# Kernel tuning notes

Measured on AMD Instinct MI355X. Metric: run time of the kernel, lower is better.

The kernel has to match this reference:

```python
import jax, jax.numpy as jnp
import numpy as np

N_NODES = 50000
N_GRAPHS = 64
IN_DIM, HIDDEN, OUT_DIM = 2063, 256, 128
E_L, E_G = 800000, 1600000


def setup_inputs() -> dict:
    key = jax.random.key(0)
    ks = jax.random.split(key, 16)
    x = jax.random.normal(ks[0], (N_NODES, IN_DIM), dtype=jnp.float32)
    edge_index_l = jax.random.randint(ks[1], (2, E_L), 0, N_NODES, dtype=jnp.int64)
    edge_index_g = jax.random.randint(ks[2], (2, E_G), 0, N_NODES, dtype=jnp.int64)
    batch = jnp.sort(jax.random.randint(ks[3], (N_NODES,), 0, N_GRAPHS, dtype=jnp.int64))

    def glorot(k, shape):
        scale = jnp.sqrt(2.0 / (shape[0] + shape[1])).astype(jnp.float32)
        return jax.random.normal(k, shape, dtype=jnp.float32) * scale

    return {
        "x": x,
        "edge_index_l": edge_index_l,
        "edge_index_g": edge_index_g,
        "batch": batch,
        "W_l1": glorot(ks[4], (IN_DIM, HIDDEN)), "b_l1": jnp.zeros((HIDDEN,), jnp.float32),
        "W_l2": glorot(ks[5], (HIDDEN, OUT_DIM)), "b_l2": jnp.zeros((OUT_DIM,), jnp.float32),
        "W_g1": glorot(ks[6], (IN_DIM, HIDDEN)), "b_g1": jnp.zeros((HIDDEN,), jnp.float32),
        "W_g2": glorot(ks[7], (HIDDEN, OUT_DIM)), "b_g2": jnp.zeros((OUT_DIM,), jnp.float32),
        "W_fuse": glorot(ks[8], (2 * OUT_DIM, OUT_DIM)), "b_fuse": jnp.zeros((OUT_DIM,), jnp.float32),
    }


def gcn_conv(x, edge_index, W, b):
    # PyG GCNConv: add self loops, symmetric D^{-1/2}(A+I)D^{-1/2} normalization,
    # linear transform then scatter-add aggregation at target nodes.
    n = x.shape[0]
    loops = jnp.arange(n, dtype=edge_index.dtype)
    src = jnp.concatenate([edge_index[0], loops])
    dst = jnp.concatenate([edge_index[1], loops])
    deg = jax.ops.segment_sum(jnp.ones_like(dst, dtype=x.dtype), dst, num_segments=n)
    dinv = jax.lax.rsqrt(deg)  # deg >= 1 due to self loops
    norm = dinv[src] * dinv[dst]  # [E+n]
    h = x @ W  # [n, out]
    msg = h[src] * norm[:, None]  # gather + scale
    return jax.ops.segment_sum(msg, dst, num_segments=n) + b


def global_mean_pool(x, batch, num_graphs):
    sums = jax.ops.segment_sum(x, batch, num_segments=num_graphs)
    cnt = jax.ops.segment_sum(jnp.ones((x.shape[0],), x.dtype), batch, num_segments=num_graphs)
    return sums / jnp.maximum(cnt, 1.0)[:, None]


def reference(x, edge_index_l, edge_index_g, batch,
              W_l1, b_l1, W_l2, b_l2, W_g1, b_g1, W_g2, b_g2, W_fuse, b_fuse):
    # dropout is identity in eval mode
    xl = jax.nn.relu(gcn_conv(x, edge_index_l, W_l1, b_l1))
    xl = gcn_conv(xl, edge_index_l, W_l2, b_l2)
    xl = global_mean_pool(xl, batch, N_GRAPHS)

    xg = jax.nn.relu(gcn_conv(x, edge_index_g, W_g1, b_g1))
    xg = gcn_conv(xg, edge_index_g, W_g2, b_g2)
    xg = global_mean_pool(xg, batch, N_GRAPHS)

    out = jnp.concatenate([xl, xg], axis=1)  # [G, 2*out_dim]
    return jax.nn.relu(out @ W_fuse + b_fuse)
```

## Files before the change

kernel.cpp:

```cpp
#include <hip/hip_runtime.h>
#include <hip/hip_bf16.h>
#include <cstdint>
#include <cstddef>


#define N_NODES 50000
#define N_GRAPHS 64
#define IN_DIM 2063
#define HIDDEN 256
#define OUT_DIM 128
#define EDGES_L 800000
#define EDGES_G 1600000
#define HCOLS 512
#define KPAD 2112
#define MPAD 50048
#define GBM 64
#define NT (KPAD / 32)
#define PCH 256
#define NCHUNK ((N_NODES + PCH - 1) / PCH)

#define QUARTER 12544
#define SL_L 64
#define SL_G 128
#define EPS 12500
#define HBLOCKS (4 * (SL_L + SL_G))

typedef __attribute__((ext_vector_type(8))) __bf16 bf16x8;
typedef __attribute__((ext_vector_type(4))) float f32x4;

__device__ __forceinline__ float bf2f(unsigned short u) {
  union { unsigned int i; float f; } c; c.i = ((unsigned int)u) << 16; return c.f;
}
__device__ __forceinline__ unsigned short f2bf(float f) {
  __hip_bfloat16 h = __float2bfloat16(f);
  return *reinterpret_cast<unsigned short*>(&h);
}

__global__ void k_cvt_w(const float* __restrict__ Wl, const float* __restrict__ Wg,
                        unsigned short* __restrict__ Wt) {
  int i = blockIdx.x * blockDim.x + threadIdx.x;
  if (i >= HCOLS * KPAD) return;
  int n = i / KPAD;
  int k = i - n * KPAD;
  float v = 0.f;
  if (k < IN_DIM) {
    v = (n < HIDDEN) ? Wl[(size_t)k * HIDDEN + n] : Wg[(size_t)k * HIDDEN + (n - HIDDEN)];
  }
  Wt[(size_t)n * KPAD + k] = f2bf(v);
}

__launch_bounds__(256)
__global__ void k_hist(const int* __restrict__ dstL, const int* __restrict__ dstG,
                       int* __restrict__ partL, int* __restrict__ partG) {
  __shared__ int hist[QUARTER];
  const int i = blockIdx.x;
  const int* __restrict__ dst;
  int slice, q;
  int* __restrict__ part;
  if (i < 4 * SL_L) {
    slice = i >> 2; q = i & 3;
    dst = dstL;
    part = partL + (size_t)(slice * 4 + q) * QUARTER;
  } else {
    int j = i - 4 * SL_L;
    slice = j >> 2; q = j & 3;
    dst = dstG;
    part = partG + (size_t)(slice * 4 + q) * QUARTER;
  }
  for (int t = threadIdx.x; t < QUARTER; t += 256) hist[t] = 0;
  __syncthreads();
  const int e0 = slice * EPS;
  const int qbase = q * QUARTER;
  for (int e = e0 + threadIdx.x; e < e0 + EPS; e += 256) {
    int d = dst[e] - qbase;
    if ((unsigned)d < QUARTER) atomicAdd(&hist[d], 1);
  }
  __syncthreads();
  for (int t = threadIdx.x; t < QUARTER; t += 256) part[t] = hist[t];
}

__global__ void k_prefix(int* __restrict__ partL, int* __restrict__ partG,
                         const int* __restrict__ batch, int* __restrict__ degL,
                         int* __restrict__ degG, float* __restrict__ dinvL,
                         float* __restrict__ dinvG, float* __restrict__ cL,
                         float* __restrict__ cG) {
  int t = blockIdx.x * blockDim.x + threadIdx.x;
  if (t >= 8 * QUARTER) return;
  const int b = t / (4 * QUARTER);
  const int n = t - b * 4 * QUARTER;
  const int q = n / QUARTER, loc = n - q * QUARTER;
  const int NS = b ? SL_G : SL_L;
  int* p = (b ? partG : partL) + (size_t)q * QUARTER + loc;
  int run = 0;
  for (int s = 0; s < NS; s++) {
    int* pp = p + (size_t)s * 4 * QUARTER;
    int v = *pp;
    *pp = run;
    run += v;
  }
  if (n < N_NODES) {
    float d = 1.0f / sqrtf((float)(run + 1));
    if (b == 0) {
      degL[n] = run; dinvL[n] = d; cL[(size_t)n * 64 + batch[n]] = d * d;
    } else {
      degG[n] = run; dinvG[n] = d; cG[(size_t)n * 64 + batch[n]] = d * d;
    }
  }
}

__global__ void k_scan1(const int* __restrict__ degL, const int* __restrict__ degG,
                        int* __restrict__ rowL, int* __restrict__ rowG,
                        const int* __restrict__ batch, int* __restrict__ start) {
  if (blockIdx.x >= 2) {
    int n = (blockIdx.x - 2) * 1024 + threadIdx.x;
    if (n >= N_NODES) return;
    int bn = batch[n];
    int bp = n ? batch[n - 1] : -1;
    for (int g = bp + 1; g <= bn; g++) start[g] = n;
    if (n == N_NODES - 1)
      for (int g = bn + 1; g <= N_GRAPHS; g++) start[g] = N_NODES;
    return;
  }
  __shared__ int part[1024];
  const int t = threadIdx.x;
  const int* __restrict__ deg = blockIdx.x ? degG : degL;
  int* __restrict__ row = blockIdx.x ? rowG : rowL;
  const int c0 = t * 49;
  int s = 0;
  for (int j = 0; j < 49; j++) {
    int idx = c0 + j;
    s += (idx < N_NODES) ? deg[idx] : 0;
  }
  part[t] = s;
  __syncthreads();
  for (int ofs = 1; ofs < 1024; ofs <<= 1) {
    int v = (t >= ofs) ? part[t - ofs] : 0;
    __syncthreads();
    part[t] += v;
    __syncthreads();
  }
  int run = (t > 0) ? part[t - 1] : 0;
  for (int j = 0; j < 49; j++) {
    int idx = c0 + j;
    if (idx < N_NODES) { row[idx] = run; run += deg[idx]; }
  }
  if (t == 1023) row[N_NODES] = part[1023];
}

__launch_bounds__(256)
__global__ void k_scatter2(const int* __restrict__ srcL, const int* __restrict__ dstL,
                           const int* __restrict__ srcG, const int* __restrict__ dstG,
                           const int* __restrict__ partL, const int* __restrict__ partG,
                           const int* __restrict__ rowL, const int* __restrict__ rowG,
                           const float* __restrict__ dinvL, const float* __restrict__ dinvG,
                           const int* __restrict__ batch, int2* __restrict__ erL,
                           int2* __restrict__ erG, float* __restrict__ cL,
                           float* __restrict__ cG) {
  __shared__ int hist[QUARTER];
  const int i = blockIdx.x;
  const int *src, *dst, *part, *row;
  const float* dinv;
  int2* er;
  float* c;
  int slice, q;
  if (i < 4 * SL_L) {
    slice = i >> 2; q = i & 3;
    src = srcL; dst = dstL; row = rowL; dinv = dinvL; er = erL; c = cL;
    part = partL + (size_t)(slice * 4 + q) * QUARTER;
  } else {
    int j = i - 4 * SL_L;
    slice = j >> 2; q = j & 3;
    src = srcG; dst = dstG; row = rowG; dinv = dinvG; er = erG; c = cG;
    part = partG + (size_t)(slice * 4 + q) * QUARTER;
  }
  for (int t = threadIdx.x; t < QUARTER; t += 256) hist[t] = 0;
  __syncthreads();
  const int e0 = slice * EPS;
  const int qbase = q * QUARTER;
  for (int e = e0 + threadIdx.x; e < e0 + EPS; e += 256) {
    int d = dst[e];
    int loc = d - qbase;
    if ((unsigned)loc < QUARTER) {
      int s = src[e];
      int rank = atomicAdd(&hist[loc], 1);
      int pos = row[d] + part[loc] + rank;
      float nrm = dinv[s] * dinv[d];
      er[pos] = make_int2(s, __float_as_int(nrm));
      atomicAdd(&c[(size_t)s * 64 + batch[d]], nrm);
    }
  }
}

__launch_bounds__(256)
__global__ void k_mfma_gemm(const float* __restrict__ X,
                            const unsigned short* __restrict__ Wt,
                            unsigned short* __restrict__ H) {
  __shared__ __align__(16) char lds[2 * 4096 + 2 * 32768];
  char* const Ab0 = lds;
  char* const Ab1 = lds + 4096;
  char* const Bb0 = lds + 8192;
  char* const Bb1 = lds + 8192 + 32768;
  const int tid = threadIdx.x;
  const int lane = tid & 63;
  const int wave = tid >> 6;
  const int brow = blockIdx.x * GBM;

  const int ar = tid >> 2;
  const int ach = tid & 3;
  const int askew = (ar >> 1) & 3;
  const int asrc = (ach ^ askew) * 8;
  const int arow_g = brow + ar;
  const bool aok = arow_g < N_NODES;
  const float* __restrict__ Arow = X + (size_t)arow_g * IN_DIM;

  const int fr = lane & 15;
  const int fq = lane >> 4;

  f32x4 acc[4][8];
  const f32x4 zero = {0.f, 0.f, 0.f, 0.f};
#pragma unroll
  for (int m = 0; m < 4; m++)
#pragma unroll
    for (int n = 0; n < 8; n++) acc[m][n] = zero;

#pragma unroll
  for (int i = 0; i < 8; i++) {
    const int s = i * 256 + tid;
    const int row = s >> 2, cch = s & 3;
    const unsigned short* g = Wt + (size_t)row * KPAD + ((cch ^ ((row >> 1) & 3)) * 8);
    __builtin_amdgcn_global_load_lds(
        (const __attribute__((address_space(1))) void*)g,
        (__attribute__((address_space(3))) void*)(Bb0 + (i * 256 + wave * 64) * 16),
        16, 0, 0);
  }
  float a[8];
#pragma unroll
  for (int j = 0; j < 8; j++) a[j] = aok ? Arow[asrc + j] : 0.f;
  {
    uint u0 = (uint)f2bf(a[0]) | ((uint)f2bf(a[1]) << 16);
    uint u1 = (uint)f2bf(a[2]) | ((uint)f2bf(a[3]) << 16);
    uint u2 = (uint)f2bf(a[4]) | ((uint)f2bf(a[5]) << 16);
    uint u3 = (uint)f2bf(a[6]) | ((uint)f2bf(a[7]) << 16);
    *(uint4*)(Ab0 + tid * 16) = make_uint4(u0, u1, u2, u3);
  }
  __syncthreads();

  for (int t = 0; t < NT; ++t) {
    const int k0 = t * 32;
    char* const Acur = (t & 1) ? Ab1 : Ab0;
    char* const Bcur = (t & 1) ? Bb1 : Bb0;
    char* const Anxt = (t & 1) ? Ab0 : Ab1;
    char* const Bnxt = (t & 1) ? Bb0 : Bb1;

    if (t + 1 < NT) {
      const int kn = k0 + 32;
#pragma unroll
      for (int i = 0; i < 8; i++) {
        const int s = i * 256 + tid;
        const int row = s >> 2, cch = s & 3;
        const unsigned short* g = Wt + (size_t)row * KPAD + kn + ((cch ^ ((row >> 1) & 3)) * 8);
        __builtin_amdgcn_global_load_lds(
            (const __attribute__((address_space(1))) void*)g,
            (__attribute__((address_space(3))) void*)(Bnxt + (i * 256 + wave * 64) * 16),
            16, 0, 0);
      }
      const int kb = kn + asrc;
      if (aok) {
        if (kb + 7 < IN_DIM) {
#pragma unroll
          for (int j = 0; j < 8; j++) a[j] = Arow[kb + j];
        } else {
#pragma unroll
          for (int j = 0; j < 8; j++) a[j] = (kb + j < IN_DIM) ? Arow[kb + j] : 0.f;
        }
      }
    }

    {
      bf16x8 bv[8];
#pragma unroll
      for (int n = 0; n < 8; n++) {
        const int row = wave * 128 + n * 16 + fr;
        bv[n] = *(const bf16x8*)(Bcur + row * 64 + ((fq ^ ((row >> 1) & 3)) * 16));
      }
#pragma unroll
      for (int m = 0; m < 4; m++) {
        const int row = m * 16 + fr;
        bf16x8 av = *(const bf16x8*)(Acur + row * 64 + ((fq ^ ((row >> 1) & 3)) * 16));
#pragma unroll
        for (int n = 0; n < 8; n++)
          acc[m][n] = __builtin_amdgcn_mfma_f32_16x16x32_bf16(av, bv[n], acc[m][n], 0, 0, 0);
      }
    }

    if (t + 1 < NT) {
      uint u0 = (uint)f2bf(a[0]) | ((uint)f2bf(a[1]) << 16);
      uint u1 = (uint)f2bf(a[2]) | ((uint)f2bf(a[3]) << 16);
      uint u2 = (uint)f2bf(a[4]) | ((uint)f2bf(a[5]) << 16);
      uint u3 = (uint)f2bf(a[6]) | ((uint)f2bf(a[7]) << 16);
      *(uint4*)(Anxt + tid * 16) = make_uint4(u0, u1, u2, u3);
    }
    __syncthreads();
  }

#pragma unroll
  for (int m = 0; m < 4; m++) {
    const int r0 = brow + m * 16 + fq * 4;
#pragma unroll
    for (int n = 0; n < 8; n++) {
      const int col = wave * 128 + n * 16 + fr;
#pragma unroll
      for (int j = 0; j < 4; j++) {
        int r = r0 + j;
        if (r < N_NODES) H[(size_t)r * HCOLS + col] = f2bf(acc[m][n][j]);
      }
    }
  }
}

__global__ void k_agg(const unsigned short* __restrict__ h,
                      const float* __restrict__ dinvL, const float* __restrict__ dinvG,
                      const int* __restrict__ rowL, const int* __restrict__ rowG,
                      const int2* __restrict__ erL, const int2* __restrict__ erG,
                      const float* __restrict__ biasL, const float* __restrict__ biasG,
                      unsigned short* __restrict__ xl) {
  const int br = blockIdx.y;
  const int node = blockIdx.x * 4 + (threadIdx.x >> 6);
  const int lane = threadIdx.x & 63;
  const float* __restrict__ dinv = br ? dinvG : dinvL;
  const int* __restrict__ rp = br ? rowG : rowL;
  const int2* __restrict__ er = br ? erG : erL;
  const float* __restrict__ bias = br ? biasG : biasL;
  const int off = br ? 256 : 0;
  const size_t lcol = off + lane * 4;

  float di = dinv[node];
  float w0 = di * di;
  ushort4 u = *(const ushort4*)(h + (size_t)node * HCOLS + lcol);
  float a0 = w0 * bf2f(u.x), a1 = w0 * bf2f(u.y), a2 = w0 * bf2f(u.z), a3 = w0 * bf2f(u.w);

  int e = rp[node];
  const int e1 = rp[node + 1];
  for (; e + 8 <= e1; e += 8) {
    int2 r[8];
    ushort4 v[8];
#pragma unroll
    for (int j = 0; j < 8; j++) r[j] = er[e + j];
#pragma unroll
    for (int j = 0; j < 8; j++)
      v[j] = *(const ushort4*)(h + (size_t)r[j].x * HCOLS + lcol);
#pragma unroll
    for (int j = 0; j < 8; j++) {
      float w = __int_as_float(r[j].y);
      a0 = fmaf(w, bf2f(v[j].x), a0);
      a1 = fmaf(w, bf2f(v[j].y), a1);
      a2 = fmaf(w, bf2f(v[j].z), a2);
      a3 = fmaf(w, bf2f(v[j].w), a3);
    }
  }
  for (; e + 4 <= e1; e += 4) {
    int2 r[4];
    ushort4 v[4];
#pragma unroll
    for (int j = 0; j < 4; j++) r[j] = er[e + j];
#pragma unroll
    for (int j = 0; j < 4; j++)
      v[j] = *(const ushort4*)(h + (size_t)r[j].x * HCOLS + lcol);
#pragma unroll
    for (int j = 0; j < 4; j++) {
      float w = __int_as_float(r[j].y);
      a0 = fmaf(w, bf2f(v[j].x), a0);
      a1 = fmaf(w, bf2f(v[j].y), a1);
      a2 = fmaf(w, bf2f(v[j].z), a2);
      a3 = fmaf(w, bf2f(v[j].w), a3);
    }
  }
  for (; e < e1; e++) {
    int2 r = er[e];
    float w = __int_as_float(r.y);
    ushort4 v = *(const ushort4*)(h + (size_t)r.x * HCOLS + lcol);
    a0 = fmaf(w, bf2f(v.x), a0);
    a1 = fmaf(w, bf2f(v.y), a1);
    a2 = fmaf(w, bf2f(v.z), a2);
    a3 = fmaf(w, bf2f(v.w), a3);
  }
  float4 b = *(const float4*)(bias + lane * 4);
  ushort4 o;
  o.x = f2bf(fmaxf(a0 + b.x, 0.f));
  o.y = f2bf(fmaxf(a1 + b.y, 0.f));
  o.z = f2bf(fmaxf(a2 + b.z, 0.f));
  o.w = f2bf(fmaxf(a3 + b.w, 0.f));
  *(ushort4*)(xl + (size_t)node * HCOLS + lcol) = o;
}

__launch_bounds__(256)
__global__ void k_pool2(const unsigned short* __restrict__ xl,
                        const float* __restrict__ cL, const float* __restrict__ cG,
                        float* __restrict__ Spart) {
  __shared__ float cs[64][64];
  const int t = threadIdx.x;
  const int chunk = blockIdx.x;
  const int br = blockIdx.y;
  const float* __restrict__ C = br ? cG : cL;
  const int xoff = br ? 256 : 0;
  const int n0 = chunk * PCH;
  float acc[64];
#pragma unroll
  for (int g = 0; g < 64; g++) acc[g] = 0.f;

  for (int tile = 0; tile < PCH; tile += 64) {
    const int base = n0 + tile;
    __syncthreads();
#pragma unroll
    for (int i = 0; i < 16; i++) {
      int idx = i * 256 + t;
      int nn = idx >> 6, gg = idx & 63;
      int node = base + nn;
      cs[nn][gg] = (node < N_NODES) ? C[(size_t)node * 64 + gg] : 0.f;
    }
    __syncthreads();
    for (int nn = 0; nn < 64; nn++) {
      int node = base + nn;
      float v = (node < N_NODES) ? bf2f(xl[(size_t)node * HCOLS + xoff + t]) : 0.f;
#pragma unroll
      for (int g4 = 0; g4 < 16; g4++) {
        float4 cv = *(const float4*)&cs[nn][g4 * 4];
        acc[g4 * 4 + 0] = fmaf(cv.x, v, acc[g4 * 4 + 0]);
        acc[g4 * 4 + 1] = fmaf(cv.y, v, acc[g4 * 4 + 1]);
        acc[g4 * 4 + 2] = fmaf(cv.z, v, acc[g4 * 4 + 2]);
        acc[g4 * 4 + 3] = fmaf(cv.w, v, acc[g4 * 4 + 3]);
      }
    }
  }
  float* sp = Spart + ((size_t)br * NCHUNK + chunk) * 16384 + t;
#pragma unroll
  for (int g = 0; g < 64; g++) sp[g * 256] = acc[g];
}

__global__ void k_pool_reduce(const float* __restrict__ Spart, float* __restrict__ S) {
  int i = blockIdx.x * blockDim.x + threadIdx.x;
  if (i >= 2 * 16384) return;
  int br = i >> 14, idx = i & 16383;
  const float* p = Spart + (size_t)br * NCHUNK * 16384 + idx;
  float s = 0.f;
  for (int ch = 0; ch < NCHUNK; ch++) s += p[(size_t)ch * 16384];
  S[i] = s;
}

__global__ void k_final(const float* __restrict__ S,
                        const float* __restrict__ Wl2, const float* __restrict__ bl2,
                        const float* __restrict__ Wg2, const float* __restrict__ bg2,
                        const float* __restrict__ Wf, const float* __restrict__ bf,
                        const int* __restrict__ start, float* __restrict__ out) {
  __shared__ float pl[OUT_DIM], pg[OUT_DIM];
  int g = blockIdx.x, t = threadIdx.x;
  float invc = 1.0f / fmaxf((float)(start[g + 1] - start[g]), 1.0f);
  const float* Sl = S + (size_t)g * HIDDEN;
  const float* Sg = S + (size_t)N_GRAPHS * HIDDEN + (size_t)g * HIDDEN;
  float al = 0.f, ag = 0.f;
  for (int k = 0; k < HIDDEN; k++) {
    al = fmaf(Sl[k], Wl2[k * OUT_DIM + t], al);
    ag = fmaf(Sg[k], Wg2[k * OUT_DIM + t], ag);
  }
  pl[t] = al * invc + bl2[t];
  pg[t] = ag * invc + bg2[t];
  __syncthreads();
  float o = bf[t];
  for (int j = 0; j < OUT_DIM; j++) {
    o = fmaf(pl[j], Wf[j * OUT_DIM + t], o);
    o = fmaf(pg[j], Wf[(OUT_DIM + j) * OUT_DIM + t], o);
  }
  out[(size_t)g * OUT_DIM + t] = fmaxf(o, 0.f);
}

extern "C" void kernel_launch(void* const* d_in, const int* in_sizes, int n_in,
                              void* d_out, int out_size, void* d_ws, size_t ws_size,
                              hipStream_t stream) {
  const float* x = (const float*)d_in[0];
  const int* el = (const int*)d_in[1];
  const int* eg = (const int*)d_in[2];
  const int* batch = (const int*)d_in[3];
  const float* Wl1 = (const float*)d_in[4];
  const float* bl1 = (const float*)d_in[5];
  const float* Wl2 = (const float*)d_in[6];
  const float* bl2 = (const float*)d_in[7];
  const float* Wg1 = (const float*)d_in[8];
  const float* bg1 = (const float*)d_in[9];
  const float* Wg2 = (const float*)d_in[10];
  const float* bg2 = (const float*)d_in[11];
  const float* Wf = (const float*)d_in[12];
  const float* bf = (const float*)d_in[13];
  float* out = (float*)d_out;
  char* ws = (char*)d_ws;

  const size_t NPAD = 200192;
  size_t off = 0;
  float* c_l = (float*)(ws + off); off += (size_t)N_NODES * 64 * 4;
  float* c_g = (float*)(ws + off); off += (size_t)N_NODES * 64 * 4;
  const size_t zero_bytes = off;
  int* start = (int*)(ws + off); off += 512;
  float* S = (float*)(ws + off); off += (size_t)2 * N_GRAPHS * HIDDEN * 4;
  int* deg_l = (int*)(ws + off); off += NPAD;
  int* deg_g = (int*)(ws + off); off += NPAD;
  float* dinv_l = (float*)(ws + off); off += NPAD;
  float* dinv_g = (float*)(ws + off); off += NPAD;
  int* row_l = (int*)(ws + off); off += NPAD;
  int* row_g = (int*)(ws + off); off += NPAD;
  int* partL = (int*)(ws + off); off += (size_t)SL_L * 4 * QUARTER * 4;
  int* partG = (int*)(ws + off); off += (size_t)SL_G * 4 * QUARTER * 4;
  int2* er_l = (int2*)(ws + off); off += (size_t)EDGES_L * 8;
  int2* er_g = (int2*)(ws + off); off += (size_t)EDGES_G * 8;
  unsigned short* Wt = (unsigned short*)(ws + off); off += (size_t)HCOLS * KPAD * 2;
  unsigned short* h = (unsigned short*)(ws + off); off += (size_t)N_NODES * HCOLS * 2;
  unsigned short* xl = (unsigned short*)(ws + off); off += (size_t)N_NODES * HCOLS * 2;
  float* Spart = (float*)partL;

  const int* srcL = el;
  const int* dstL = el + EDGES_L;
  const int* srcG = eg;
  const int* dstG = eg + EDGES_G;

  hipMemsetAsync(ws, 0, zero_bytes, stream);

  k_cvt_w<<<(HCOLS * KPAD + 255) / 256, 256, 0, stream>>>(Wl1, Wg1, Wt);

  k_hist<<<HBLOCKS, 256, 0, stream>>>(dstL, dstG, partL, partG);
  k_prefix<<<(8 * QUARTER + 255) / 256, 256, 0, stream>>>(partL, partG, batch, deg_l, deg_g,
                                                          dinv_l, dinv_g, c_l, c_g);
  k_scan1<<<51, 1024, 0, stream>>>(deg_l, deg_g, row_l, row_g, batch, start);
  k_scatter2<<<HBLOCKS, 256, 0, stream>>>(srcL, dstL, srcG, dstG, partL, partG, row_l, row_g,
                                          dinv_l, dinv_g, batch, er_l, er_g, c_l, c_g);

  k_mfma_gemm<<<MPAD / GBM, 256, 0, stream>>>(x, Wt, h);

  dim3 agrid(N_NODES / 4, 2);
  k_agg<<<agrid, 256, 0, stream>>>(h, dinv_l, dinv_g, row_l, row_g, er_l, er_g, bl1, bg1, xl);

  dim3 pgrid(NCHUNK, 2);
  k_pool2<<<pgrid, 256, 0, stream>>>(xl, c_l, c_g, Spart);
  k_pool_reduce<<<(2 * 16384 + 255) / 256, 256, 0, stream>>>(Spart, S);

  k_final<<<N_GRAPHS, OUT_DIM, 0, stream>>>(S, Wl2, bl2, Wg2, bg2, Wf, bf, start, out);
}
```

Baseline: 950.8 us.

## Merge edge scatter and MFMA GEMM into one interleaved heterogeneous launch

Fuses the CSR edge-scatter kernel and the bf16 MFMA feature GEMM into a single launch. The first 2*HBLOCKS blocks alternate between scatter and GEMM work, and the remaining blocks do GEMM, so the latency-bound scatter atomics can overlap with the compute-bound GEMM on the same CUs. The scatter blocks now reserve the GEMM's larger LDS allocation, which can reduce their occupancy. The scatter path and the GEMM path also share one register budget.

```diff
diff --git a/kernel.cpp b/kernel.cpp
--- a/kernel.cpp
+++ b/kernel.cpp
@@ -15,6 +15,7 @@
 #define KPAD 2112
 #define MPAD 50048
 #define GBM 64
+#define NGB (MPAD / GBM)
 #define NT (KPAD / 32)
 #define PCH 256
 #define NCHUNK ((N_NODES + PCH - 1) / PCH)
@@ -148,54 +149,66 @@
 }
 
 __launch_bounds__(256)
-__global__ void k_scatter2(const int* __restrict__ srcL, const int* __restrict__ dstL,
-                           const int* __restrict__ srcG, const int* __restrict__ dstG,
-                           const int* __restrict__ partL, const int* __restrict__ partG,
-                           const int* __restrict__ rowL, const int* __restrict__ rowG,
-                           const float* __restrict__ dinvL, const float* __restrict__ dinvG,
-                           const int* __restrict__ batch, int2* __restrict__ erL,
-                           int2* __restrict__ erG, float* __restrict__ cL,
-                           float* __restrict__ cG) {
-  __shared__ int hist[QUARTER];
-  const int i = blockIdx.x;
-  const int *src, *dst, *part, *row;
-  const float* dinv;
-  int2* er;
-  float* c;
-  int slice, q;
-  if (i < 4 * SL_L) {
-    slice = i >> 2; q = i & 3;
-    src = srcL; dst = dstL; row = rowL; dinv = dinvL; er = erL; c = cL;
-    part = partL + (size_t)(slice * 4 + q) * QUARTER;
+__global__ void k_gemm_scat(const float* __restrict__ X,
+                            const unsigned short* __restrict__ Wt,
+                            unsigned short* __restrict__ H,
+                            const int* __restrict__ srcL, const int* __restrict__ dstL,
+                            const int* __restrict__ srcG, const int* __restrict__ dstG,
+                            const int* __restrict__ partL, const int* __restrict__ partG,
+                            const int* __restrict__ rowL, const int* __restrict__ rowG,
+                            const float* __restrict__ dinvL, const float* __restrict__ dinvG,
+                            const int* __restrict__ batch, int2* __restrict__ erL,
+                            int2* __restrict__ erG, float* __restrict__ cL,
+                            float* __restrict__ cG) {
+  __shared__ __align__(16) char lds[2 * 4096 + 2 * 32768];
+  const int b = blockIdx.x;
+  bool isGemm;
+  int rid;
+  if (b < 2 * HBLOCKS) {
+    isGemm = (b & 1) == 0;
+    rid = b >> 1;
   } else {
-    int j = i - 4 * SL_L;
-    slice = j >> 2; q = j & 3;
-    src = srcG; dst = dstG; row = rowG; dinv = dinvG; er = erG; c = cG;
-    part = partG + (size_t)(slice * 4 + q) * QUARTER;
-  }
-  for (int t = threadIdx.x; t < QUARTER; t += 256) hist[t] = 0;
-  __syncthreads();
-  const int e0 = slice * EPS;
-  const int qbase = q * QUARTER;
-  for (int e = e0 + threadIdx.x; e < e0 + EPS; e += 256) {
-    int d = dst[e];
-    int loc = d - qbase;
-    if ((unsigned)loc < QUARTER) {
-      int s = src[e];
-      int rank = atomicAdd(&hist[loc], 1);
-      int pos = row[d] + part[loc] + rank;
-      float nrm = dinv[s] * dinv[d];
-      er[pos] = make_int2(s, __float_as_int(nrm));
-      atomicAdd(&c[(size_t)s * 64 + batch[d]], nrm);
-    }
-  }
-}
-
-__launch_bounds__(256)
-__global__ void k_mfma_gemm(const float* __restrict__ X,
-                            const unsigned short* __restrict__ Wt,
-                            unsigned short* __restrict__ H) {
-  __shared__ __align__(16) char lds[2 * 4096 + 2 * 32768];
+    isGemm = true;
+    rid = HBLOCKS + (b - 2 * HBLOCKS);
+  }
+
+  if (!isGemm) {
+    int* hist = (int*)lds;
+    const int i = rid;
+    const int *src, *dst, *part, *row;
+    const float* dinv;
+    int2* er;
+    float* c;
+    int slice, q;
+    if (i < 4 * SL_L) {
+      slice = i >> 2; q = i & 3;
+      src = srcL; dst = dstL; row = rowL; dinv = dinvL; er = erL; c = cL;
+      part = partL + (size_t)(slice * 4 + q) * QUARTER;
+    } else {
+      int j = i - 4 * SL_L;
+      slice = j >> 2; q = j & 3;
+      src = srcG; dst = dstG; row = rowG; dinv = dinvG; er = erG; c = cG;
+      part = partG + (size_t)(slice * 4 + q) * QUARTER;
+    }
+    for (int t = threadIdx.x; t < QUARTER; t += 256) hist[t] = 0;
+    __syncthreads();
+    const int e0 = slice * EPS;
+    const int qbase = q * QUARTER;
+    for (int e = e0 + threadIdx.x; e < e0 + EPS; e += 256) {
+      int d = dst[e];
+      int loc = d - qbase;
+      if ((unsigned)loc < QUARTER) {
+        int s = src[e];
+        int rank = atomicAdd(&hist[loc], 1);
+        int pos = row[d] + part[loc] + rank;
+        float nrm = dinv[s] * dinv[d];
+        er[pos] = make_int2(s, __float_as_int(nrm));
+        atomicAdd(&c[(size_t)s * 64 + batch[d]], nrm);
+      }
+    }
+    return;
+  }
+
   char* const Ab0 = lds;
   char* const Ab1 = lds + 4096;
   char* const Bb0 = lds + 8192;
@@ -203,7 +216,7 @@
   const int tid = threadIdx.x;
   const int lane = tid & 63;
   const int wave = tid >> 6;
-  const int brow = blockIdx.x * GBM;
+  const int brow = rid * GBM;
 
   const int ar = tid >> 2;
   const int ach = tid & 3;
@@ -528,10 +541,10 @@
   k_prefix<<<(8 * QUARTER + 255) / 256, 256, 0, stream>>>(partL, partG, batch, deg_l, deg_g,
                                                           dinv_l, dinv_g, c_l, c_g);
   k_scan1<<<51, 1024, 0, stream>>>(deg_l, deg_g, row_l, row_g, batch, start);
-  k_scatter2<<<HBLOCKS, 256, 0, stream>>>(srcL, dstL, srcG, dstG, partL, partG, row_l, row_g,
-                                          dinv_l, dinv_g, batch, er_l, er_g, c_l, c_g);
-
-  k_mfma_gemm<<<MPAD / GBM, 256, 0, stream>>>(x, Wt, h);
+
+  k_gemm_scat<<<NGB + HBLOCKS, 256, 0, stream>>>(x, Wt, h, srcL, dstL, srcG, dstG,
+                                                 partL, partG, row_l, row_g, dinv_l, dinv_g,
+                                                 batch, er_l, er_g, c_l, c_g);
 
   dim3 agrid(N_NODES / 4, 2);
   k_agg<<<agrid, 256, 0, stream>>>(h, dinv_l, dinv_g, row_l, row_g, er_l, er_g, bl1, bg1, xl);
```

Result: slower. 1.026 ms (+8.0%).
